# Kernel optimization log

Measured on AMD Instinct MI355X. Metric: run time of the kernel, lower is better.

Reference implementation:

```python
import jax, jax.numpy as jnp
import numpy as np

B, N, H, HD = 32, 256, 6, 32            # windows, tokens/window (16x16), heads, head_dim
C = H * HD                               # dim = 192
TOPK_IN, TOPK_OUT = 64, 32               # incoming pfa topk, num_topk[layer_id]
NBIAS = (2 * 16 - 1) ** 2                # relative-position bias table size = 961
SCALE = HD ** -0.5
EPS = 1e-20


def setup_inputs() -> dict:
    key = jax.random.key(0)
    ks = jax.random.split(key, 7)
    qkvp = jax.random.normal(ks[0], (B, N, 4 * C), dtype=jnp.float32)
    pfa_values = jax.random.uniform(ks[1], (B, H, N, TOPK_IN), dtype=jnp.float32)
    pfa_index = jax.random.randint(ks[2], (B, H, N, TOPK_IN), 0, N, dtype=jnp.int64)
    rpi = jax.random.randint(ks[3], (N, N), 0, NBIAS, dtype=jnp.int64)
    rpb_table = 0.02 * jax.random.normal(ks[4], (NBIAS, H), dtype=jnp.float32)
    proj_w = 0.02 * jax.random.normal(ks[5], (C, C), dtype=jnp.float32)
    proj_b = jnp.zeros((C,), dtype=jnp.float32)
    return {"qkvp": qkvp, "pfa_values": pfa_values, "pfa_index": pfa_index,
            "rpi": rpi, "rpb_table": rpb_table, "proj_w": proj_w, "proj_b": proj_b}


def _gather_rows(x, idx):
    # x: [b, h, n, d], idx: [b, h, n, t] -> [b, h, n, t, d] = x[b, h, idx[b,h,n,t], :]
    return jnp.take_along_axis(x[:, :, None, :, :], idx[..., None], axis=3)


def reference(qkvp, pfa_values, pfa_index, rpi, rpb_table, proj_w, proj_b):
    b_, n, c4 = qkvp.shape
    c = c4 // 4
    hd = c // H
    qkvp = qkvp.reshape(b_, n, 4, H, hd).transpose(2, 0, 3, 1, 4)  # [4, b, h, n, hd]
    q, k, v, v_lepe = qkvp[0], qkvp[1], qkvp[2], qkvp[3]
    q = q * SCALE

    # sparse QK^T over gathered keys: attn[b,h,i,t] = <q[b,h,i], k[b,h,idx[b,h,i,t]]>
    k_sel = _gather_rows(k, pfa_index)                      # [b, h, n, TOPK_IN, hd]
    attn = jnp.einsum('bhnd,bhntd->bhnt', q, k_sel)

    # relative position bias, gathered along the sparse key index
    rpb = rpb_table[rpi.reshape(-1)].reshape(n, n, H).transpose(2, 0, 1)  # [h, n, n]
    bias = jnp.take_along_axis(jnp.broadcast_to(rpb[None], (b_, H, n, n)),
                               pfa_index, axis=-1)           # [b, h, n, TOPK_IN]
    attn = attn + bias

    attn = jax.nn.softmax(attn, axis=-1)

    # progressive focusing: modulate by previous attn values and renormalize
    attn = attn * pfa_values
    denom = attn.sum(axis=-1, keepdims=True)
    attn = (attn + EPS) / (denom + EPS)

    # prune to self.topk = TOPK_OUT entries and remap indices
    topv, topi = jax.lax.top_k(attn, TOPK_OUT)               # [b, h, n, TOPK_OUT]
    new_index = jnp.take_along_axis(pfa_index, topi, axis=-1)

    # sparse attn @ V over gathered values, plus LePE residual
    v_sel = _gather_rows(v, new_index)                       # [b, h, n, TOPK_OUT, hd]
    x = jnp.einsum('bhnt,bhntd->bhnd', topv, v_sel) + v_lepe
    x = x.transpose(0, 2, 1, 3).reshape(b_, n, c)
    x = x @ proj_w.T + proj_b
    return x, topv, new_index
```

## Files before the change

kernel.cpp:

```cpp
#include <hip/hip_runtime.h>

#define B_    32
#define N_    256
#define H_    6
#define HD_   32
#define C_    192
#define C4_   768
#define TKIN  64
#define TKOUT 32
#define WULP  32u

__global__ __launch_bounds__(256) void attn_topk_kernel(
    const float* __restrict__ qkvp,
    const float* __restrict__ pfa_values,
    const int*   __restrict__ pfa_index,
    const int*   __restrict__ rpi,
    const float* __restrict__ rpb_table,
    float* __restrict__ x_pre,
    float* __restrict__ out_topv,
    float* __restrict__ out_nidx)
{
    const int lane  = threadIdx.x & 63;
    const int wslot = threadIdx.x >> 6;

    const int n  = blockIdx.x;
    const int x  = n & 7;
    const int r  = n >> 3;
    const int bq = r / 384;
    const int wb = r - bq * 384;
    const int b  = x * 4 + bq;
    const int row = b * (H_ * N_) + wb * 4 + wslot;

    const int rem = row - b * (H_ * N_);
    const int h   = rem / N_;
    const int i   = rem - h * N_;

    const int row_off = row * TKIN;
    const int idx  = pfa_index[row_off + lane];
    const float pv = pfa_values[row_off + lane];

    __shared__ uint2  s_pk[4][64];
    __shared__ double s_k64[4][64];
    __shared__ float  s_a[4][TKOUT];
    __shared__ int    s_i[4][TKOUT];

    const float* qp = qkvp + (size_t)(b * N_ + i) * C4_ + h * HD_;
    const float* kp = qkvp + (size_t)(b * N_ + idx) * C4_ + C_ + h * HD_;
    const float bias = rpb_table[rpi[i * N_ + idx] * H_ + h];

    float acc;
    {
        #pragma clang fp contract(off)
        const float SC = 0.17677669529663687f;
        acc = 0.f;
        for (int d = 0; d < HD_; ++d) {
            const float qd   = qp[d] * SC;
            const float prod = qd * kp[d];
            acc = acc + prod;
        }
        acc = acc + bias;
    }

    float m = acc;
    #pragma unroll
    for (int s = 32; s; s >>= 1) m = fmaxf(m, __shfl_xor(m, s));

    float e;
    {
        #pragma clang fp contract(off)
        const float t = acc - m;
        e = (float)exp((double)t);
    }

    float ssum;
    {
        #pragma clang fp contract(off)
        float y = e, r2 = e;
        #pragma unroll
        for (int k = 1; k < 8; ++k) { y = __shfl_down(y, 8); r2 = r2 + y; }
        const float t1 = r2 + __shfl_xor(r2, 1);
        const float t2 = t1 + __shfl_xor(t1, 2);
        const float t3 = t2 + __shfl_xor(t2, 4);
        ssum = __shfl(t3, 0);
    }

    float w;
    {
        #pragma clang fp contract(off)
        const float s32 = e / ssum;
        w = s32 * pv;
    }

    float denom;
    {
        #pragma clang fp contract(off)
        float y = w, r2 = w;
        #pragma unroll
        for (int k = 1; k < 8; ++k) { y = __shfl_down(y, 8); r2 = r2 + y; }
        const float t1 = r2 + __shfl_xor(r2, 1);
        const float t2 = t1 + __shfl_xor(t1, 2);
        const float t3 = t2 + __shfl_xor(t2, 4);
        denom = __shfl(t3, 0);
    }

    float a32;
    {
        #pragma clang fp contract(off)
        a32 = (w + 1e-20f) / (denom + 1e-20f);
    }

    const unsigned abits = __float_as_uint(a32);
    const unsigned long long myK =
        ((unsigned long long)abits << 6) | (unsigned long long)(63 - lane);
    s_pk[wslot][lane] = make_uint2((unsigned)myK, (unsigned)(myK >> 32));

    int rank = 0;
    #pragma unroll
    for (int j = 0; j < 64; ++j) {
        const uint2 kj = s_pk[wslot][j];
        const unsigned long long K =
            ((unsigned long long)kj.y << 32) | (unsigned long long)kj.x;
        rank += (K > myK);
    }

    {
        const int sorted = __builtin_amdgcn_ds_permute(rank << 2, (int)abits);
        const int nxt    = __shfl_down(sorted, 1);
        const unsigned gap = (unsigned)sorted - (unsigned)nxt;
        const bool nearf = (lane < 63) && (gap <= WULP);
        if (__any(nearf)) {
            double acc64 = 0.0;
            #pragma unroll
            for (int d0 = 0; d0 < 8; ++d0) {
                const float4 q4 = *(const float4*)(qp + 4 * d0);
                const float4 k4 = *(const float4*)(kp + 4 * d0);
                acc64 = fma((double)q4.x, (double)k4.x, acc64);
                acc64 = fma((double)q4.y, (double)k4.y, acc64);
                acc64 = fma((double)q4.z, (double)k4.z, acc64);
                acc64 = fma((double)q4.w, (double)k4.w, acc64);
            }
            acc64 = acc64 * 0.17677669529663687 + (double)bias;
            const double okey = exp(acc64) * (double)pv;
            s_k64[wslot][lane] = okey;

            rank = 0;
            #pragma unroll
            for (int j = 0; j < 64; ++j) {
                const uint2 kj = s_pk[wslot][j];
                const unsigned kbits = (kj.y << 26) | (kj.x >> 6);
                const float  kj32 = __uint_as_float(kbits);
                const double kj64 = s_k64[wslot][j];
                const bool tie  = (kj32 == a32);
                const bool lt64 = (kj64 < okey);
                const bool gt64 = (kj64 > okey);
                const bool eq64 = (kj64 == okey);
                const bool before = tie ? (lt64 || (eq64 && j < lane))
                                        : (gt64 || (eq64 && kj32 > a32));
                rank += before;
            }
        }
    }

    if (rank < TKOUT) {
        const size_t obase = (size_t)row * TKOUT + rank;
        out_topv[obase] = a32;
        out_nidx[obase] = (float)idx;
        s_a[wslot][rank] = a32;
        s_i[wslot][rank] = idx;
    }

    const int d    = lane & 31;
    const int half = lane >> 5;
    float xd = 0.f;
    #pragma unroll
    for (int s16 = 0; s16 < 16; ++s16) {
        const int sI = half * 16 + s16;
        const float av = s_a[wslot][sI];
        const int   vi = s_i[wslot][sI];
        xd += av * qkvp[(size_t)(b * N_ + vi) * C4_ + 2 * C_ + h * HD_ + d];
    }
    xd += __shfl_xor(xd, 32);
    if (half == 0) {
        const float lepe = qkvp[(size_t)(b * N_ + i) * C4_ + 3 * C_ + h * HD_ + d];
        x_pre[(size_t)(b * N_ + i) * C_ + h * HD_ + d] = xd + lepe;
    }
}

#define TB_ 8
__global__ __launch_bounds__(192) void proj_kernel(
    const float* __restrict__ x_pre,
    const float* __restrict__ w,
    const float* __restrict__ bias,
    float* __restrict__ out)
{
    __shared__ float xs[TB_ * C_];
    const int o    = threadIdx.x;
    const int tok0 = blockIdx.x * TB_;

    #pragma unroll
    for (int r = 0; r < TB_; ++r)
        xs[r * C_ + o] = x_pre[(size_t)(tok0 + r) * C_ + o];
    __syncthreads();

    float accv[TB_];
    #pragma unroll
    for (int t = 0; t < TB_; ++t) accv[t] = 0.f;

    const float* wrow = w + (size_t)o * C_;
    for (int c = 0; c < C_; c += 4) {
        const float4 wv = *(const float4*)(wrow + c);
        #pragma unroll
        for (int t = 0; t < TB_; ++t) {
            const float4 xv = *(const float4*)(&xs[t * C_ + c]);
            accv[t] += xv.x * wv.x + xv.y * wv.y + xv.z * wv.z + xv.w * wv.w;
        }
    }
    const float bo = bias[o];
    #pragma unroll
    for (int t = 0; t < TB_; ++t)
        out[(size_t)(tok0 + t) * C_ + o] = accv[t] + bo;
}

extern "C" void kernel_launch(void* const* d_in, const int* in_sizes, int n_in,
                              void* d_out, int out_size, void* d_ws, size_t ws_size,
                              hipStream_t stream) {
    const float* qkvp       = (const float*)d_in[0];
    const float* pfa_values = (const float*)d_in[1];
    const int*   pfa_index  = (const int*)d_in[2];
    const int*   rpi        = (const int*)d_in[3];
    const float* rpb_table  = (const float*)d_in[4];
    const float* proj_w     = (const float*)d_in[5];
    const float* proj_b     = (const float*)d_in[6];

    float* out = (float*)d_out;
    float* out_x    = out;
    float* out_topv = out + (size_t)B_ * N_ * C_;
    float* out_nidx = out_topv + (size_t)B_ * H_ * N_ * TKOUT;

    float* x_pre = (float*)d_ws;

    const int rows = B_ * H_ * N_;
    attn_topk_kernel<<<rows / 4, 256, 0, stream>>>(
        qkvp, pfa_values, pfa_index, rpi, rpb_table, x_pre, out_topv, out_nidx);

    const int ntok = B_ * N_;
    proj_kernel<<<ntok / TB_, 192, 0, stream>>>(x_pre, proj_w, proj_b, out_x);
}
```

Baseline: 114.3 us.

## Rank by fp64 key first and compute exact fp32 softmax only on near ties

The primary path now computes the unnormalized fp64 score exp(qk+bias)*pv and ranks on its bits, with the output value taken as okey/dsum. The fp32 softmax emulation, with its max, sum and denominator reductions, runs only when some pair of adjacent sorted keys lies within a small gap of the upper fp64 bits. This swaps the per-row fp32 chain for an fp64 dot product, which may be slow on this hardware. It also changes the output value (okey/dsum instead of the bit-exact fp32 a32) on the fast path, so results may differ slightly from the reference.

Measured after the change: 114.4 us. About the same (+0.1%).

```diff
diff --git a/kernel.cpp b/kernel.cpp
--- a/kernel.cpp
+++ b/kernel.cpp
@@ -8,7 +8,7 @@
 #define C4_   768
 #define TKIN  64
 #define TKOUT 32
-#define WULP  32u
+#define GAP32 4u
 
 __global__ __launch_bounds__(256) void attn_topk_kernel(
     const float* __restrict__ qkvp,
@@ -40,6 +40,7 @@
     const float pv = pfa_values[row_off + lane];
 
     __shared__ uint2  s_pk[4][64];
+    __shared__ float  s_k32[4][64];
     __shared__ double s_k64[4][64];
     __shared__ float  s_a[4][TKOUT];
     __shared__ int    s_i[4][TKOUT];
@@ -48,70 +49,19 @@
     const float* kp = qkvp + (size_t)(b * N_ + idx) * C4_ + C_ + h * HD_;
     const float bias = rpb_table[rpi[i * N_ + idx] * H_ + h];
 
-    float acc;
-    {
-        #pragma clang fp contract(off)
-        const float SC = 0.17677669529663687f;
-        acc = 0.f;
-        for (int d = 0; d < HD_; ++d) {
-            const float qd   = qp[d] * SC;
-            const float prod = qd * kp[d];
-            acc = acc + prod;
-        }
-        acc = acc + bias;
-    }
-
-    float m = acc;
-    #pragma unroll
-    for (int s = 32; s; s >>= 1) m = fmaxf(m, __shfl_xor(m, s));
-
-    float e;
-    {
-        #pragma clang fp contract(off)
-        const float t = acc - m;
-        e = (float)exp((double)t);
-    }
-
-    float ssum;
-    {
-        #pragma clang fp contract(off)
-        float y = e, r2 = e;
-        #pragma unroll
-        for (int k = 1; k < 8; ++k) { y = __shfl_down(y, 8); r2 = r2 + y; }
-        const float t1 = r2 + __shfl_xor(r2, 1);
-        const float t2 = t1 + __shfl_xor(t1, 2);
-        const float t3 = t2 + __shfl_xor(t2, 4);
-        ssum = __shfl(t3, 0);
-    }
-
-    float w;
-    {
-        #pragma clang fp contract(off)
-        const float s32 = e / ssum;
-        w = s32 * pv;
-    }
-
-    float denom;
-    {
-        #pragma clang fp contract(off)
-        float y = w, r2 = w;
-        #pragma unroll
-        for (int k = 1; k < 8; ++k) { y = __shfl_down(y, 8); r2 = r2 + y; }
-        const float t1 = r2 + __shfl_xor(r2, 1);
-        const float t2 = t1 + __shfl_xor(t1, 2);
-        const float t3 = t2 + __shfl_xor(t2, 4);
-        denom = __shfl(t3, 0);
-    }
-
-    float a32;
-    {
-        #pragma clang fp contract(off)
-        a32 = (w + 1e-20f) / (denom + 1e-20f);
-    }
-
-    const unsigned abits = __float_as_uint(a32);
-    const unsigned long long myK =
-        ((unsigned long long)abits << 6) | (unsigned long long)(63 - lane);
+    double acc64 = 0.0;
+    for (int d = 0; d < HD_; ++d)
+        acc64 = fma((double)qp[d], (double)kp[d], acc64);
+    acc64 = acc64 * 0.17677669529663687 + (double)bias;
+    const double okey = exp(acc64) * (double)pv;
+
+    double dsum = okey;
+    #pragma unroll
+    for (int s = 32; s; s >>= 1) dsum += __shfl_xor(dsum, s);
+
+    union { double d; unsigned long long u; } ou; ou.d = okey;
+    const unsigned long long ob = ou.u;
+    const unsigned long long myK = (ob & ~63ull) | (unsigned long long)(63 - lane);
     s_pk[wslot][lane] = make_uint2((unsigned)myK, (unsigned)(myK >> 32));
 
     int rank = 0;
@@ -123,49 +73,95 @@
         rank += (K > myK);
     }
 
-    {
-        const int sorted = __builtin_amdgcn_ds_permute(rank << 2, (int)abits);
-        const int nxt    = __shfl_down(sorted, 1);
-        const unsigned gap = (unsigned)sorted - (unsigned)nxt;
-        const bool nearf = (lane < 63) && (gap <= WULP);
-        if (__any(nearf)) {
-            double acc64 = 0.0;
+    const unsigned otop = (unsigned)(ob >> 32);
+    const int sorted = __builtin_amdgcn_ds_permute(rank << 2, (int)otop);
+    const int nxt    = __shfl_down(sorted, 1);
+    const unsigned gap = (unsigned)sorted - (unsigned)nxt;
+    const bool nearf = (lane < 63) && (gap <= GAP32);
+
+    float outval;
+    if (__any(nearf)) {
+        float acc;
+        {
+            #pragma clang fp contract(off)
+            const float SC = 0.17677669529663687f;
+            acc = 0.f;
+            for (int d = 0; d < HD_; ++d) {
+                const float qd   = qp[d] * SC;
+                const float prod = qd * kp[d];
+                acc = acc + prod;
+            }
+            acc = acc + bias;
+        }
+        float m = acc;
+        #pragma unroll
+        for (int s = 32; s; s >>= 1) m = fmaxf(m, __shfl_xor(m, s));
+        float e;
+        {
+            #pragma clang fp contract(off)
+            const float t = acc - m;
+            e = (float)exp((double)t);
+        }
+        float ssum;
+        {
+            #pragma clang fp contract(off)
+            float y = e, r2 = e;
             #pragma unroll
-            for (int d0 = 0; d0 < 8; ++d0) {
-                const float4 q4 = *(const float4*)(qp + 4 * d0);
-                const float4 k4 = *(const float4*)(kp + 4 * d0);
-                acc64 = fma((double)q4.x, (double)k4.x, acc64);
-                acc64 = fma((double)q4.y, (double)k4.y, acc64);
-                acc64 = fma((double)q4.z, (double)k4.z, acc64);
-                acc64 = fma((double)q4.w, (double)k4.w, acc64);
-            }
-            acc64 = acc64 * 0.17677669529663687 + (double)bias;
-            const double okey = exp(acc64) * (double)pv;
-            s_k64[wslot][lane] = okey;
-
-            rank = 0;
+            for (int k = 1; k < 8; ++k) { y = __shfl_down(y, 8); r2 = r2 + y; }
+            const float t1 = r2 + __shfl_xor(r2, 1);
+            const float t2 = t1 + __shfl_xor(t1, 2);
+            const float t3 = t2 + __shfl_xor(t2, 4);
+            ssum = __shfl(t3, 0);
+        }
+        float w;
+        {
+            #pragma clang fp contract(off)
+            const float s32 = e / ssum;
+            w = s32 * pv;
+        }
+        float denom;
+        {
+            #pragma clang fp contract(off)
+            float y = w, r2 = w;
             #pragma unroll
-            for (int j = 0; j < 64; ++j) {
-                const uint2 kj = s_pk[wslot][j];
-                const unsigned kbits = (kj.y << 26) | (kj.x >> 6);
-                const float  kj32 = __uint_as_float(kbits);
-                const double kj64 = s_k64[wslot][j];
-                const bool tie  = (kj32 == a32);
-                const bool lt64 = (kj64 < okey);
-                const bool gt64 = (kj64 > okey);
-                const bool eq64 = (kj64 == okey);
-                const bool before = tie ? (lt64 || (eq64 && j < lane))
-                                        : (gt64 || (eq64 && kj32 > a32));
-                rank += before;
-            }
-        }
+            for (int k = 1; k < 8; ++k) { y = __shfl_down(y, 8); r2 = r2 + y; }
+            const float t1 = r2 + __shfl_xor(r2, 1);
+            const float t2 = t1 + __shfl_xor(t1, 2);
+            const float t3 = t2 + __shfl_xor(t2, 4);
+            denom = __shfl(t3, 0);
+        }
+        float a32;
+        {
+            #pragma clang fp contract(off)
+            a32 = (w + 1e-20f) / (denom + 1e-20f);
+        }
+
+        s_k32[wslot][lane] = a32;
+        s_k64[wslot][lane] = okey;
+
+        rank = 0;
+        #pragma unroll
+        for (int j = 0; j < 64; ++j) {
+            const float  kj32 = s_k32[wslot][j];
+            const double kj64 = s_k64[wslot][j];
+            const bool tie  = (kj32 == a32);
+            const bool lt64 = (kj64 < okey);
+            const bool gt64 = (kj64 > okey);
+            const bool eq64 = (kj64 == okey);
+            const bool before = tie ? (lt64 || (eq64 && j < lane))
+                                    : (gt64 || (eq64 && kj32 > a32));
+            rank += before;
+        }
+        outval = a32;
+    } else {
+        outval = (float)(okey / dsum);
     }
 
     if (rank < TKOUT) {
         const size_t obase = (size_t)row * TKOUT + rank;
-        out_topv[obase] = a32;
+        out_topv[obase] = outval;
         out_nidx[obase] = (float)idx;
-        s_a[wslot][rank] = a32;
+        s_a[wslot][rank] = outval;
         s_i[wslot][rank] = idx;
     }
 
```
